# Kernel optimization log

Measured on AMD Instinct MI355X. Metric: run time of the kernel, lower is better.

The kernel has to match this reference:

```python
import jax, jax.numpy as jnp
import numpy as np

B, INPUT_DIM, N_NEURONS, NEURON_DIM, N_STEPS = 16384, 256, 32, 128, 3


def setup_inputs() -> dict:
    key = jax.random.key(0)
    ks = jax.random.split(key, 9)
    d, n, di = NEURON_DIM, N_NEURONS, INPUT_DIM
    return {
        "x": jax.random.normal(ks[0], (B, di), dtype=jnp.float32),
        "W_in": jax.random.normal(ks[1], (di, d), dtype=jnp.float32) / np.sqrt(di),
        "b_in": jax.random.normal(ks[2], (d,), dtype=jnp.float32) * 0.01,
        "neuron_states": jax.random.normal(ks[3], (n, d), dtype=jnp.float32),
        "edge_vectors": jax.random.normal(ks[4], (n, n, d), dtype=jnp.float32),
        "W_rec": jax.random.normal(ks[5], (d, di), dtype=jnp.float32) / np.sqrt(d),
        "b_rec": jax.random.normal(ks[6], (di,), dtype=jnp.float32) * 0.01,
        "W_score": jax.random.normal(ks[7], (d, 1), dtype=jnp.float32) / np.sqrt(d),
        "b_score": jax.random.normal(ks[8], (1,), dtype=jnp.float32) * 0.01,
    }


def reference(x, W_in, b_in, neuron_states, edge_vectors, W_rec, b_rec, W_score, b_score):
    # x: (B, input_dim)
    x_t = x @ W_in + b_in                                  # (B, d)
    states = neuron_states[None, :, :] + x_t[:, None, :]   # (B, n, d)
    n = neuron_states.shape[0]
    off_diag = (1.0 - jnp.eye(n, dtype=states.dtype))      # zero self-messages (i != j)
    for _ in range(N_STEPS):
        # score[b,i,j] = e_ij . states[b,i]
        scores = jnp.einsum('ijq,biq->bij', edge_vectors, states) * off_diag
        # new_states[b,i,p] = sum_j score[b,i,j] * states[b,j,p]
        states = jax.nn.relu(jnp.einsum('bij,bjp->bip', scores, states))
    out = states[:, -1]                                    # last neuron's state (B, d)
    recreation = out @ W_rec + b_rec                       # (B, input_dim)
    score_out = out @ W_score + b_score                    # (B, 1)
    return (recreation, score_out)
```

## Files before the change

kernel.cpp:

```cpp
#include <hip/hip_runtime.h>
#include <cstdint>


#define BTOT 16384
#define NBATCH 15
#define ROWB 272
#define STB  8720
#define ST(b) ((b) * STB)
#define SC_BASE 130800
#define SC_BS 2080
#define SC(b) (SC_BASE + (b) * SC_BS)
#define SIGF_OFF 162000
#define LDS_TOTAL 162064

#define WS_EH    0
#define WS_WINT  262144
#define WS_WRECT 327680
#define WS_NSMX  393216
#define WS_NSMN  393728
#define WS_XT    394240
#define WS_NEED  4654080

typedef _Float16 f16;
typedef _Float16 f16x8 __attribute__((ext_vector_type(8)));
typedef float f32x4 __attribute__((ext_vector_type(4)));
typedef unsigned int u32x4 __attribute__((ext_vector_type(4)));
typedef unsigned int u32x2 __attribute__((ext_vector_type(2)));

union H8 { u32x4 u; f16x8 h; };
union H4 { u32x2 u; f16 h[4]; };

__device__ __forceinline__ float exp2i(int e) {
    return __uint_as_float((unsigned)(e + 127) << 23);
}
__device__ __forceinline__ int flog2(float m) {
    return (int)((__float_as_uint(m) >> 23) & 0xFF) - 127;
}

__global__ void agm_conv(const float* __restrict__ edge, const float* __restrict__ W_in,
                         const float* __restrict__ W_rec, const float* __restrict__ ns,
                         f16* __restrict__ edge_h, f16* __restrict__ W_inT,
                         f16* __restrict__ W_recT, float* __restrict__ nsmax,
                         float* __restrict__ nsmin)
{
    const int tid = blockIdx.x * 256 + threadIdx.x;
    {
        const int i = tid >> 12, j = (tid >> 7) & 31;
        float v = edge[tid];
        if (i == j) v = 0.f;
        edge_h[tid] = (f16)v;
    }
    if (tid < 32768) {
        const int c = tid >> 8, k = tid & 255;
        W_inT[tid] = (f16)W_in[k * 128 + c];
    }
    if (tid < 32768) {
        const int n = tid >> 7, p = tid & 127;
        W_recT[tid] = (f16)W_rec[p * 256 + n];
    }
    if (tid < 128) {
        float mx = -1e30f, mn = 1e30f;
        for (int i = 0; i < 32; ++i) {
            const float v = ns[i * 128 + tid];
            mx = fmaxf(mx, v); mn = fminf(mn, v);
        }
        nsmax[tid] = mx; nsmin[tid] = mn;
    }
}

__global__ __launch_bounds__(256)
void agm_xt(const float* __restrict__ x, const f16* __restrict__ W_inT,
            const float* __restrict__ b_in, f16* __restrict__ xt)
{
    const int tid = threadIdx.x;
    const int w = tid >> 6, ln = tid & 63, g = ln >> 4, c15 = ln & 15;
    const int bt = blockIdx.x;
    const size_t brow = (size_t)(bt * 16 + c15) * 256;
    H8 A[8];
    #pragma unroll
    for (int ks = 0; ks < 8; ++ks) {
        const float4 pa = *(const float4*)(x + brow + ks * 32 + g * 8);
        const float4 pb = *(const float4*)(x + brow + ks * 32 + g * 8 + 4);
        A[ks].h = (f16x8){(f16)pa.x,(f16)pa.y,(f16)pa.z,(f16)pa.w,
                          (f16)pb.x,(f16)pb.y,(f16)pb.z,(f16)pb.w};
    }
    #pragma unroll
    for (int nt = 0; nt < 2; ++nt) {
        const int col = w * 32 + nt * 16 + c15;
        f32x4 d = {0,0,0,0};
        #pragma unroll
        for (int ks = 0; ks < 8; ++ks) {
            H8 b;
            b.u = *(const u32x4*)(W_inT + col * 256 + ks * 32 + g * 8);
            d = __builtin_amdgcn_mfma_f32_16x16x32_f16(A[ks].h, b.h, d, 0, 0, 0);
        }
        const float bc = b_in[col];
        #pragma unroll
        for (int r = 0; r < 4; ++r)
            xt[(size_t)(bt * 16 + g * 4 + r) * 128 + col] = (f16)(d[r] + bc);
    }
}

__global__ __launch_bounds__(1024, 4)
void agm_main(const f16* __restrict__ xto, const float* __restrict__ ns,
              const float* __restrict__ nsmax, const float* __restrict__ nsmin,
              const f16* __restrict__ edge_h, const f16* __restrict__ W_recT,
              const float* __restrict__ b_rec, const float* __restrict__ W_score,
              const float* __restrict__ b_score,
              float* __restrict__ out_rec, float* __restrict__ out_sc)
{
    __shared__ __align__(16) char smem[LDS_TOTAL];
    const int tid = threadIdx.x;
    const int w   = tid >> 6;
    const int ln  = tid & 63;
    const int g   = ln >> 4;
    const int c15 = ln & 15;
    const long bg0 = (long)blockIdx.x * NBATCH;

    int sig = 0;

    if (w < NBATCH) {
        long bgw = bg0 + w;
        if (bgw >= BTOT) bgw = BTOT - 1;
        const float xt0 = (float)xto[(size_t)bgw * 128 + ln];
        const float xt1 = (float)xto[(size_t)bgw * 128 + 64 + ln];
        float m = fmaxf(fmaxf(fabsf(nsmax[ln] + xt0),      fabsf(nsmin[ln] + xt0)),
                        fmaxf(fabsf(nsmax[ln + 64] + xt1), fabsf(nsmin[ln + 64] + xt1)));
        m = fmaxf(m, 1e-30f);
        m = fmaxf(m, __shfl_xor(m, 1));
        m = fmaxf(m, __shfl_xor(m, 2));
        m = fmaxf(m, __shfl_xor(m, 4));
        m = fmaxf(m, __shfl_xor(m, 8));
        m = fmaxf(m, __shfl_xor(m, 16));
        m = fmaxf(m, __shfl_xor(m, 32));
        sig = 10 - flog2(m);
        const float s0 = exp2i(sig);
        #pragma unroll 4
        for (int i = 0; i < 32; ++i) {
            *(f16*)(smem + ST(w) + i*ROWB + ln*2) =
                (f16)((ns[i*128 + ln] + xt0) * s0);
            *(f16*)(smem + ST(w) + i*ROWB + (ln + 64)*2) =
                (f16)((ns[i*128 + 64 + ln] + xt1) * s0);
        }
    }
    __syncthreads();

    for (int t = 0; t < 3; ++t) {
        if (t < 2) {
            const int bb = c15 < NBATCH ? c15 : NBATCH - 1;
            #pragma unroll
            for (int ii = 0; ii < 2; ++ii) {
                const int i = w * 2 + ii;
                H8 Bf[4];
                #pragma unroll
                for (int ks = 0; ks < 4; ++ks)
                    Bf[ks].u = *(const u32x4*)(smem + ST(bb) + i*ROWB + (ks*32 + g*8)*2);
                f32x4 d0 = {0,0,0,0}, d1 = {0,0,0,0};
                #pragma unroll
                for (int ks = 0; ks < 4; ++ks) {
                    H8 A0, A1;
                    A0.u = *(const u32x4*)(edge_h + ((i*32 + c15)*128 + ks*32 + g*8));
                    A1.u = *(const u32x4*)(edge_h + ((i*32 + c15)*128 + 2048 + ks*32 + g*8));
                    if (i == c15)      A0.u = (u32x4){0,0,0,0};
                    if (i == 16 + c15) A1.u = (u32x4){0,0,0,0};
                    d0 = __builtin_amdgcn_mfma_f32_16x16x32_f16(A0.h, Bf[ks].h, d0, 0, 0, 0);
                    d1 = __builtin_amdgcn_mfma_f32_16x16x32_f16(A1.h, Bf[ks].h, d1, 0, 0, 0);
                }
                if (c15 < NBATCH) {
                    char* scb = smem + SC(c15) + i * 64;
                    H4 p0, p1;
                    #pragma unroll
                    for (int r = 0; r < 4; ++r) {
                        p0.h[r] = (f16)(d0[r] * 0x1p-8f);
                        p1.h[r] = (f16)(d1[r] * 0x1p-8f);
                    }
                    *(u32x2*)(scb + g*8)      = p0.u;
                    *(u32x2*)(scb + 32 + g*8) = p1.u;
                }
            }
        } else if (w == 15) {
            const int i = 31;
            const int bb = c15 < NBATCH ? c15 : NBATCH - 1;
            H8 Bf[4];
            #pragma unroll
            for (int ks = 0; ks < 4; ++ks)
                Bf[ks].u = *(const u32x4*)(smem + ST(bb) + i*ROWB + (ks*32 + g*8)*2);
            f32x4 d0 = {0,0,0,0}, d1 = {0,0,0,0};
            #pragma unroll
            for (int ks = 0; ks < 4; ++ks) {
                H8 A0, A1;
                A0.u = *(const u32x4*)(edge_h + ((i*32 + c15)*128 + ks*32 + g*8));
                A1.u = *(const u32x4*)(edge_h + ((i*32 + c15)*128 + 2048 + ks*32 + g*8));
                if (i == 16 + c15) A1.u = (u32x4){0,0,0,0};
                d0 = __builtin_amdgcn_mfma_f32_16x16x32_f16(A0.h, Bf[ks].h, d0, 0, 0, 0);
                d1 = __builtin_amdgcn_mfma_f32_16x16x32_f16(A1.h, Bf[ks].h, d1, 0, 0, 0);
            }
            if (c15 < NBATCH) {
                char* scb = smem + SC(c15) + i * 64;
                H4 p0, p1;
                #pragma unroll
                for (int r = 0; r < 4; ++r) {
                    p0.h[r] = (f16)(d0[r] * 0x1p-8f);
                    p1.h[r] = (f16)(d1[r] * 0x1p-8f);
                }
                *(u32x2*)(scb + g*8)      = p0.u;
                *(u32x2*)(scb + 32 + g*8) = p1.u;
            }
        }
        __syncthreads();

        if (w < NBATCH) {
            const int bb = w;
            char* scb = smem + SC(bb);
            if (t < 2) {
                H8 alo, ahi;
                alo.u = *(const u32x4*)(scb + c15*64 + g*16);
                ahi.u = *(const u32x4*)(scb + 1024 + c15*64 + g*16);
                float rs0 = 0.f, rs1 = 0.f;
                #pragma unroll
                for (int r = 0; r < 8; ++r) {
                    rs0 += fabsf((float)alo.h[r]);
                    rs1 += fabsf((float)ahi.h[r]);
                }
                rs0 += __shfl_xor(rs0, 16);  rs0 += __shfl_xor(rs0, 32);
                rs1 += __shfl_xor(rs1, 16);  rs1 += __shfl_xor(rs1, 32);
                float rmax = fmaxf(fmaxf(rs0, rs1), 1e-10f);
                rmax = fmaxf(rmax, __shfl_xor(rmax, 1));
                rmax = fmaxf(rmax, __shfl_xor(rmax, 2));
                rmax = fmaxf(rmax, __shfl_xor(rmax, 4));
                rmax = fmaxf(rmax, __shfl_xor(rmax, 8));
                int ge = 9 - flog2(rmax * 2048.0f);
                if (ge > 60) ge = 60;
                if (ge < -60) ge = -60;
                sig = 2 * sig - 8 + ge;
                const float gs = exp2i(ge);
                #pragma unroll
                for (int pt = 0; pt < 8; ++pt) {
                    H8 bf;
                    #pragma unroll
                    for (int jj = 0; jj < 8; ++jj)
                        bf.h[jj] = *(const f16*)(smem + ST(bb) + (g*8 + jj)*ROWB
                                                 + (pt*16 + c15)*2);
                    const f32x4 z = {0,0,0,0};
                    f32x4 dlo = __builtin_amdgcn_mfma_f32_16x16x32_f16(alo.h, bf.h, z, 0, 0, 0);
                    f32x4 dhi = __builtin_amdgcn_mfma_f32_16x16x32_f16(ahi.h, bf.h, z, 0, 0, 0);
                    const int p = pt*16 + c15;
                    #pragma unroll
                    for (int r = 0; r < 4; ++r) {
                        const int il = g*4 + r, ih = il + 16;
                        *(f16*)(smem + ST(bb) + il*ROWB + p*2) =
                            (f16)(fmaxf(dlo[r], 0.f) * gs);
                        *(f16*)(smem + ST(bb) + ih*ROWB + p*2) =
                            (f16)(fmaxf(dhi[r], 0.f) * gs);
                    }
                }
            } else {
                H8 ahi;
                ahi.u = *(const u32x4*)(scb + 1024 + c15*64 + g*16);
                float rs1 = 0.f;
                #pragma unroll
                for (int r = 0; r < 8; ++r) rs1 += fabsf((float)ahi.h[r]);
                rs1 += __shfl_xor(rs1, 16);  rs1 += __shfl_xor(rs1, 32);
                float rmax = fmaxf(rs1, 1e-10f);
                rmax = fmaxf(rmax, __shfl_xor(rmax, 1));
                rmax = fmaxf(rmax, __shfl_xor(rmax, 2));
                rmax = fmaxf(rmax, __shfl_xor(rmax, 4));
                rmax = fmaxf(rmax, __shfl_xor(rmax, 8));
                int ge = 9 - flog2(rmax * 2048.0f);
                if (ge > 60) ge = 60;
                if (ge < -60) ge = -60;
                sig = 2 * sig - 8 + ge;
                const float gs = exp2i(ge);
                #pragma unroll
                for (int pt = 0; pt < 8; ++pt) {
                    H8 bf;
                    #pragma unroll
                    for (int jj = 0; jj < 8; ++jj)
                        bf.h[jj] = *(const f16*)(smem + ST(bb) + (g*8 + jj)*ROWB
                                                 + (pt*16 + c15)*2);
                    const f32x4 z = {0,0,0,0};
                    f32x4 dhi = __builtin_amdgcn_mfma_f32_16x16x32_f16(ahi.h, bf.h, z, 0, 0, 0);
                    if (g == 3)
                        *(f16*)(scb + (pt*16 + c15)*2) =
                            (f16)(fmaxf(dhi[3], 0.f) * gs);
                }
                if (ln == 0) ((int*)(smem + SIGF_OFF))[bb] = sig;
            }
        }
        __syncthreads();
    }

    {
        const int* sigf = (const int*)(smem + SIGF_OFF);
        const int bbx = c15 < NBATCH ? c15 : NBATCH - 1;
        H8 A[4];
        #pragma unroll
        for (int ks = 0; ks < 4; ++ks)
            A[ks].u = *(const u32x4*)(smem + SC(bbx) + (ks*32 + g*8)*2);
        float dsc[4];
        #pragma unroll
        for (int r = 0; r < 4; ++r) {
            const int batch = g*4 + r;
            int e = -(batch < NBATCH ? sigf[batch] : 0);
            if (e > 126) e = 126; if (e < -126) e = -126;
            dsc[r] = exp2i(e);
        }
        {
            const int col = w * 16 + c15;
            f32x4 d = {0,0,0,0};
            #pragma unroll
            for (int ks = 0; ks < 4; ++ks) {
                H8 b;
                b.u = *(const u32x4*)(W_recT + col*128 + ks*32 + g*8);
                d = __builtin_amdgcn_mfma_f32_16x16x32_f16(A[ks].h, b.h, d, 0, 0, 0);
            }
            const float bc = b_rec[col];
            #pragma unroll
            for (int r = 0; r < 4; ++r) {
                const int batch = g*4 + r;
                if (batch < NBATCH && bg0 + batch < BTOT)
                    out_rec[(bg0 + batch)*256 + col] = d[r]*dsc[r] + bc;
            }
        }
        if (w < NBATCH && bg0 + w < BTOT) {
            const char* ob = smem + SC(w);
            float v = (float)(*(const f16*)(ob + ln*2)) * W_score[ln]
                    + (float)(*(const f16*)(ob + (ln + 64)*2)) * W_score[ln + 64];
            v += __shfl_xor(v, 1);
            v += __shfl_xor(v, 2);
            v += __shfl_xor(v, 4);
            v += __shfl_xor(v, 8);
            v += __shfl_xor(v, 16);
            v += __shfl_xor(v, 32);
            int e = -sig;
            if (e > 126) e = 126; if (e < -126) e = -126;
            if (ln == 0) out_sc[bg0 + w] = v * exp2i(e) + b_score[0];
        }
    }
}

__global__ __launch_bounds__(256, 2)
void agm_fb(const float* __restrict__ x, const float* __restrict__ W_in,
            const float* __restrict__ b_in, const float* __restrict__ ns,
            const float* __restrict__ edge, const float* __restrict__ W_rec,
            const float* __restrict__ b_rec, const float* __restrict__ W_score,
            const float* __restrict__ b_score, float* __restrict__ out_rec,
            float* __restrict__ out_sc)
{
    __shared__ float st[4][32][128];
    const int t = threadIdx.x;
    const int b = __builtin_amdgcn_readfirstlane(t >> 6);
    const int ln = t & 63;
    const long bg = (long)blockIdx.x * 4 + b;
    {
        const float* xb = x + bg * 256;
        float a0 = b_in[ln], a1 = b_in[ln + 64];
        for (int k = 0; k < 256; k += 4) {
            const float4 xv = *(const float4*)(xb + k);
            a0 += xv.x * W_in[(k+0)*128 + ln];  a1 += xv.x * W_in[(k+0)*128 + 64 + ln];
            a0 += xv.y * W_in[(k+1)*128 + ln];  a1 += xv.y * W_in[(k+1)*128 + 64 + ln];
            a0 += xv.z * W_in[(k+2)*128 + ln];  a1 += xv.z * W_in[(k+2)*128 + 64 + ln];
            a0 += xv.w * W_in[(k+3)*128 + ln];  a1 += xv.w * W_in[(k+3)*128 + 64 + ln];
        }
        for (int i = 0; i < 32; ++i) {
            st[b][i][ln]      = ns[i*128 + ln]      + a0;
            st[b][i][ln + 64] = ns[i*128 + 64 + ln] + a1;
        }
    }
    __syncthreads();
    const int h = ln >> 5, q4 = ln & 31;
    for (int step = 0; step < 2; ++step) {
        float acc0[32], acc1[32];
        #pragma unroll
        for (int i = 0; i < 32; ++i) { acc0[i] = 0.f; acc1[i] = 0.f; }
        for (int j = 0; j < 32; ++j) {
            const float s0 = st[b][j][ln], s1 = st[b][j][ln + 64];
            #pragma unroll
            for (int m = 0; m < 16; ++m) {
                const int i = 2*m + h;
                const float4 ev = *(const float4*)(edge + (((size_t)(i*32 + j)) << 7) + (q4 << 2));
                const float4 sv = *(const float4*)(&st[b][i][q4 << 2]);
                float s = ev.x*sv.x + ev.y*sv.y + ev.z*sv.z + ev.w*sv.w;
                s += __shfl_xor(s, 1); s += __shfl_xor(s, 2); s += __shfl_xor(s, 4);
                s += __shfl_xor(s, 8); s += __shfl_xor(s, 16);
                float c0 = __shfl(s, 0), c1 = __shfl(s, 32);
                if (2*m == j) c0 = 0.f;
                if (2*m + 1 == j) c1 = 0.f;
                acc0[2*m] += c0*s0; acc1[2*m] += c0*s1;
                acc0[2*m+1] += c1*s0; acc1[2*m+1] += c1*s1;
            }
            __syncthreads();
        }
        #pragma unroll
        for (int i = 0; i < 32; ++i) {
            st[b][i][ln]      = fmaxf(acc0[i], 0.f);
            st[b][i][ln + 64] = fmaxf(acc1[i], 0.f);
        }
        __syncthreads();
    }
    {
        float o0 = 0.f, o1 = 0.f;
        #pragma unroll
        for (int m = 0; m < 16; ++m) {
            const int jj = 2*m + h;
            const float4 ev = *(const float4*)(edge + (((size_t)(31*32 + jj)) << 7) + (q4 << 2));
            const float4 sv = *(const float4*)(&st[b][31][q4 << 2]);
            float s = ev.x*sv.x + ev.y*sv.y + ev.z*sv.z + ev.w*sv.w;
            s += __shfl_xor(s, 1); s += __shfl_xor(s, 2); s += __shfl_xor(s, 4);
            s += __shfl_xor(s, 8); s += __shfl_xor(s, 16);
            float c0 = __shfl(s, 0), c1 = __shfl(s, 32);
            if (2*m == 31) c0 = 0.f;
            if (2*m + 1 == 31) c1 = 0.f;
            o0 += c0*st[b][2*m][ln] + c1*st[b][2*m+1][ln];
            o1 += c0*st[b][2*m][ln+64] + c1*st[b][2*m+1][ln+64];
        }
        __syncthreads();
        st[b][0][ln] = fmaxf(o0, 0.f);
        st[b][0][ln + 64] = fmaxf(o1, 0.f);
    }
    __syncthreads();
    {
        const float* ob = &st[b][0][0];
        float r0 = b_rec[ln], r1 = b_rec[ln+64], r2 = b_rec[ln+128], r3 = b_rec[ln+192];
        for (int p = 0; p < 128; ++p) {
            const float ov = ob[p];
            r0 += ov * W_rec[p*256 + ln];       r1 += ov * W_rec[p*256 + 64 + ln];
            r2 += ov * W_rec[p*256 + 128 + ln]; r3 += ov * W_rec[p*256 + 192 + ln];
        }
        float* orow = out_rec + bg * 256;
        orow[ln] = r0; orow[ln+64] = r1; orow[ln+128] = r2; orow[ln+192] = r3;
        float s = ob[ln]*W_score[ln] + ob[ln+64]*W_score[ln+64];
        s += __shfl_xor(s, 32); s += __shfl_xor(s, 16); s += __shfl_xor(s, 8);
        s += __shfl_xor(s, 4);  s += __shfl_xor(s, 2);  s += __shfl_xor(s, 1);
        if (ln == 0) out_sc[bg] = s + b_score[0];
    }
}

extern "C" void kernel_launch(void* const* d_in, const int* in_sizes, int n_in,
                              void* d_out, int out_size, void* d_ws, size_t ws_size,
                              hipStream_t stream) {
    const float* x     = (const float*)d_in[0];
    const float* W_in  = (const float*)d_in[1];
    const float* bin   = (const float*)d_in[2];
    const float* ns    = (const float*)d_in[3];
    const float* edge  = (const float*)d_in[4];
    const float* W_rec = (const float*)d_in[5];
    const float* brec  = (const float*)d_in[6];
    const float* W_sc  = (const float*)d_in[7];
    const float* b_sc  = (const float*)d_in[8];
    (void)n_in;

    const int B = in_sizes[0] / 256;
    float* out = (float*)d_out;
    float* outsc = out + (size_t)B * 256;

    if (ws_size < (size_t)WS_NEED) {
        agm_fb<<<dim3(B / 4), dim3(256), 0, stream>>>(
            x, W_in, bin, ns, edge, W_rec, brec, W_sc, b_sc, out, outsc);
        return;
    }

    char* ws = (char*)d_ws;
    f16*   edge_h = (f16*)(ws + WS_EH);
    f16*   W_inT  = (f16*)(ws + WS_WINT);
    f16*   W_recT = (f16*)(ws + WS_WRECT);
    float* nsmax  = (float*)(ws + WS_NSMX);
    float* nsmin  = (float*)(ws + WS_NSMN);
    f16*   xto    = (f16*)(ws + WS_XT);

    agm_conv<<<dim3(512), dim3(256), 0, stream>>>(edge, W_in, W_rec, ns,
                                                  edge_h, W_inT, W_recT, nsmax, nsmin);
    agm_xt<<<dim3(B / 16), dim3(256), 0, stream>>>(x, W_inT, bin, xto);
    const int nblk = (B + NBATCH - 1) / NBATCH;
    agm_main<<<dim3(nblk), dim3(1024), 0, stream>>>(xto, ns, nsmax, nsmin, edge_h,
                                                    W_recT, brec, W_sc, b_sc,
                                                    out, outsc);
}
```

Measured before the change: 189.1 us.

## Pack 16 batches per block to fill MFMA columns and drop row padding

Raises the batches per block from 15 to 16 so every column of the 16-wide MFMA tiles carries real work. This removes the clamping and predicate logic for the unused lane and cuts the grid to B/16 blocks. The LDS row padding is removed to keep the larger tile within the shared-memory budget, and the per-batch scale exponent now lives inside each score buffer. The cost is that unpadded 256-byte rows may cause LDS bank conflicts on the strided column reads. Batch sizes not divisible by 16 now go to the fallback kernel.

```diff
diff --git a/kernel.cpp b/kernel.cpp
--- a/kernel.cpp
+++ b/kernel.cpp
@@ -3,15 +3,14 @@
 
 
 #define BTOT 16384
-#define NBATCH 15
-#define ROWB 272
-#define STB  8720
+#define NBATCH 16
+#define ROWB 256
+#define STB  8192
 #define ST(b) ((b) * STB)
-#define SC_BASE 130800
-#define SC_BS 2080
+#define SC_BASE 131072
+#define SC_BS 2048
 #define SC(b) (SC_BASE + (b) * SC_BS)
-#define SIGF_OFF 162000
-#define LDS_TOTAL 162064
+#define LDS_TOTAL 163840
 
 #define WS_EH    0
 #define WS_WINT  262144
@@ -119,9 +118,8 @@
 
     int sig = 0;
 
-    if (w < NBATCH) {
-        long bgw = bg0 + w;
-        if (bgw >= BTOT) bgw = BTOT - 1;
+    {
+        const long bgw = bg0 + w;
         const float xt0 = (float)xto[(size_t)bgw * 128 + ln];
         const float xt1 = (float)xto[(size_t)bgw * 128 + 64 + ln];
         float m = fmaxf(fmaxf(fabsf(nsmax[ln] + xt0),      fabsf(nsmin[ln] + xt0)),
@@ -147,7 +145,7 @@
 
     for (int t = 0; t < 3; ++t) {
         if (t < 2) {
-            const int bb = c15 < NBATCH ? c15 : NBATCH - 1;
+            const int bb = c15;
             #pragma unroll
             for (int ii = 0; ii < 2; ++ii) {
                 const int i = w * 2 + ii;
@@ -166,7 +164,7 @@
                     d0 = __builtin_amdgcn_mfma_f32_16x16x32_f16(A0.h, Bf[ks].h, d0, 0, 0, 0);
                     d1 = __builtin_amdgcn_mfma_f32_16x16x32_f16(A1.h, Bf[ks].h, d1, 0, 0, 0);
                 }
-                if (c15 < NBATCH) {
+                {
                     char* scb = smem + SC(c15) + i * 64;
                     H4 p0, p1;
                     #pragma unroll
@@ -178,9 +176,9 @@
                     *(u32x2*)(scb + 32 + g*8) = p1.u;
                 }
             }
-        } else if (w == 15) {
+        } else if (w == 0) {
             const int i = 31;
-            const int bb = c15 < NBATCH ? c15 : NBATCH - 1;
+            const int bb = c15;
             H8 Bf[4];
             #pragma unroll
             for (int ks = 0; ks < 4; ++ks)
@@ -195,7 +193,7 @@
                 d0 = __builtin_amdgcn_mfma_f32_16x16x32_f16(A0.h, Bf[ks].h, d0, 0, 0, 0);
                 d1 = __builtin_amdgcn_mfma_f32_16x16x32_f16(A1.h, Bf[ks].h, d1, 0, 0, 0);
             }
-            if (c15 < NBATCH) {
+            {
                 char* scb = smem + SC(c15) + i * 64;
                 H4 p0, p1;
                 #pragma unroll
@@ -209,7 +207,7 @@
         }
         __syncthreads();
 
-        if (w < NBATCH) {
+        {
             const int bb = w;
             char* scb = smem + SC(bb);
             if (t < 2) {
@@ -284,24 +282,22 @@
                         *(f16*)(scb + (pt*16 + c15)*2) =
                             (f16)(fmaxf(dhi[3], 0.f) * gs);
                 }
-                if (ln == 0) ((int*)(smem + SIGF_OFF))[bb] = sig;
+                if (ln == 0) *(int*)(scb + 256) = sig;
             }
         }
         __syncthreads();
     }
 
     {
-        const int* sigf = (const int*)(smem + SIGF_OFF);
-        const int bbx = c15 < NBATCH ? c15 : NBATCH - 1;
         H8 A[4];
         #pragma unroll
         for (int ks = 0; ks < 4; ++ks)
-            A[ks].u = *(const u32x4*)(smem + SC(bbx) + (ks*32 + g*8)*2);
+            A[ks].u = *(const u32x4*)(smem + SC(c15) + (ks*32 + g*8)*2);
         float dsc[4];
         #pragma unroll
         for (int r = 0; r < 4; ++r) {
             const int batch = g*4 + r;
-            int e = -(batch < NBATCH ? sigf[batch] : 0);
+            int e = -*(const int*)(smem + SC(batch) + 256);
             if (e > 126) e = 126; if (e < -126) e = -126;
             dsc[r] = exp2i(e);
         }
@@ -318,11 +314,10 @@
             #pragma unroll
             for (int r = 0; r < 4; ++r) {
                 const int batch = g*4 + r;
-                if (batch < NBATCH && bg0 + batch < BTOT)
-                    out_rec[(bg0 + batch)*256 + col] = d[r]*dsc[r] + bc;
-            }
-        }
-        if (w < NBATCH && bg0 + w < BTOT) {
+                out_rec[(bg0 + batch)*256 + col] = d[r]*dsc[r] + bc;
+            }
+        }
+        {
             const char* ob = smem + SC(w);
             float v = (float)(*(const f16*)(ob + ln*2)) * W_score[ln]
                     + (float)(*(const f16*)(ob + (ln + 64)*2)) * W_score[ln + 64];
@@ -454,7 +449,7 @@
     float* out = (float*)d_out;
     float* outsc = out + (size_t)B * 256;
 
-    if (ws_size < (size_t)WS_NEED) {
+    if (ws_size < (size_t)WS_NEED || (B % NBATCH) != 0) {
         agm_fb<<<dim3(B / 4), dim3(256), 0, stream>>>(
             x, W_in, bin, ns, edge, W_rec, brec, W_sc, b_sc, out, outsc);
         return;
@@ -471,7 +466,7 @@
     agm_conv<<<dim3(512), dim3(256), 0, stream>>>(edge, W_in, W_rec, ns,
                                                   edge_h, W_inT, W_recT, nsmax, nsmin);
     agm_xt<<<dim3(B / 16), dim3(256), 0, stream>>>(x, W_inT, bin, xto);
-    const int nblk = (B + NBATCH - 1) / NBATCH;
+    const int nblk = B / NBATCH;
     agm_main<<<dim3(nblk), dim3(1024), 0, stream>>>(xto, ns, nsmax, nsmin, edge_h,
                                                     W_recT, brec, W_sc, b_sc,
                                                     out, outsc);
```

New measurement: 155.9 us (median of 2 runs). 1.21x faster.
